# Optimization experiments

Measured on AMD Instinct MI355X. Metric: run time of the kernel, lower is better.

Reference implementation:

```python
import jax, jax.numpy as jnp
import numpy as np


def setup_inputs() -> dict:
    B, L, D, M, S = 4, 1024, 1024, 16, 8
    key = jax.random.key(0)
    ks = jax.random.split(key, 12)
    sd = 0.02
    inp = {
        "hid": jax.random.normal(ks[0], (B, L, D), jnp.float32),
        "src_hid": jax.random.normal(ks[1], (B, L, D), jnp.float32),
        "sp_width": jax.random.randint(ks[2], (B, L), 0, 9),
        "max_sp_len": S,
        "attention_mask": jnp.ones((B, L), bool),
        "src_mask": jnp.ones((B, L), bool),
        # span-start attention (1 head): query/key linears + relative-key embedding table
        "wq_st": sd * jax.random.normal(ks[3], (D, D), jnp.float32),
        "bq_st": jnp.zeros((D,), jnp.float32),
        "wk_st": sd * jax.random.normal(ks[4], (D, D), jnp.float32),
        "bk_st": jnp.zeros((D,), jnp.float32),
        "rel_st": sd * jax.random.normal(ks[5], (2 * M + 1, D), jnp.float32),
        # span-end attention
        "wq_ed": sd * jax.random.normal(ks[6], (D, D), jnp.float32),
        "bq_ed": jnp.zeros((D,), jnp.float32),
        "wk_ed": sd * jax.random.normal(ks[7], (D, D), jnp.float32),
        "bk_ed": jnp.zeros((D,), jnp.float32),
        "rel_ed": sd * jax.random.normal(ks[8], (2 * M + 1, D), jnp.float32),
        # sp_emb: Linear(2D -> D), stored as [2D, D] (x @ W + b)
        "sp_w": sd * jax.random.normal(ks[9], (2 * D, D), jnp.float32),
        "sp_b": jnp.zeros((D,), jnp.float32),
    }
    return inp


def reference(hid, src_hid, sp_width, max_sp_len, attention_mask, src_mask,
              wq_st, bq_st, wk_st, bk_st, rel_st,
              wq_ed, bq_ed, wk_ed, bk_ed, rel_ed, sp_w, sp_b):
    B, L, D = hid.shape
    scale = 1.0 / jnp.sqrt(jnp.float32(D))
    M = (rel_st.shape[0] - 1) // 2
    pos = jnp.arange(L)
    rel_idx = jnp.clip(pos[None, :] - pos[:, None], -M, M) + M          # [L,L]
    rel_idx_b = jnp.broadcast_to(rel_idx[None], (B, L, L))

    amask = (src_mask[:, :, None] & attention_mask[:, None, :]).astype(jnp.float32)  # [B,Lq,Lk]
    attn_w0 = amask / jnp.clip(jnp.sum(amask, 2, keepdims=True), 1e-6)

    def attn(query, wq, bq, wk, bk, rel_tab, mask):
        # single-head relative-position attention; returns attention weights [B,L,L]
        q = (query @ wq + bq) * scale                                   # [B,L,D]
        k = hid @ wk + bk                                               # [B,L,D]
        sc = jnp.einsum('bqd,bkd->bqk', q, k)
        # q . rel_emb[rel_idx[q_pos,k_pos]]: contract with table then gather (avoids [L,L,D])
        rel_sc = jnp.take_along_axis(jnp.einsum('bqd,rd->bqr', q, rel_tab), rel_idx_b, axis=2)
        sc = jnp.where(mask > 0, sc + rel_sc, -1e18)
        return jax.nn.softmax(sc, axis=-1)

    def upd(attn_w, hidp):
        # weighted sum of hid + linear + relu (dropout is identity in eval)
        hidc = jnp.einsum('bqk,bkd->bqd', attn_w, hid)
        return jax.nn.relu(jnp.concatenate([hidp, hidc], axis=2) @ sp_w + sp_b)

    sts, eds, masks = [attn_w0], [attn_w0], []
    hid1, hid2 = src_hid, src_hid
    for i in range(max_sp_len):
        m = (i < sp_width).astype(jnp.float32)                          # [B,L]
        masks.append(m)
        mask_i = m[:, :, None] * amask                                  # [B,L,L]
        hid1 = upd(sts[-1], hid1)
        sts.append(attn(hid1, wq_st, bq_st, wk_st, bk_st, rel_st, mask_i))
        hid2 = upd(eds[-1], hid2)
        eds.append(attn(hid2, wq_ed, bq_ed, wk_ed, bk_ed, rel_ed, mask_i))

    return (jnp.stack(sts[1:], -2),   # [B,L,S,L]
            jnp.stack(eds[1:], -2),   # [B,L,S,L]
            jnp.stack(masks, -1))     # [B,L,S]
```

## Files before the change

### kernel.cpp

```cpp
#include <hip/hip_runtime.h>

typedef unsigned short u16;
typedef __attribute__((ext_vector_type(8))) short bh8;
typedef __attribute__((ext_vector_type(4))) float f4;

__device__ __forceinline__ u16 f2b(float x){
  union { float f; unsigned u; } c; c.f = x;
  unsigned r = (c.u + 0x7FFFu + ((c.u >> 16) & 1u)) >> 16;
  return (u16)r;
}
__device__ __forceinline__ float b2f(u16 h){
  union { unsigned u; float f; } c; c.u = ((unsigned)h) << 16; return c.f;
}
__device__ __forceinline__ void gload16(const void* g, void* l){
  __builtin_amdgcn_global_load_lds((const __attribute__((address_space(1))) void*)g,
                                   (__attribute__((address_space(3))) void*)l, 16, 0, 0);
}


__global__ __launch_bounds__(256) void convall_k(const float* __restrict__ hid,
                                                 const float* __restrict__ wq0, const float* __restrict__ wq1,
                                                 const float* __restrict__ wk0, const float* __restrict__ wk1,
                                                 u16* __restrict__ hidB, u16* __restrict__ wqB, u16* __restrict__ wkB){
  long i = (long)blockIdx.x*256 + threadIdx.x;
  const float* src; u16* dst; long off;
  if      (i < 4194304L){ src = hid; dst = hidB;           off = i; }
  else if (i < 5242880L){ src = wq0; dst = wqB;            off = i - 4194304L; }
  else if (i < 6291456L){ src = wq1; dst = wqB + 1048576;  off = i - 5242880L; }
  else if (i < 7340032L){ src = wk0; dst = wkB;            off = i - 6291456L; }
  else                  { src = wk1; dst = wkB + 1048576;  off = i - 7340032L; }
  dst[off] = f2b(src[off]);
}

__global__ __launch_bounds__(256) void uniform_k(const int* __restrict__ spw, float* __restrict__ out){
  int blk = blockIdx.x;
  int s = blk >> 12, bl = blk & 4095;
  int w = spw[bl];
  if (w >= 8) return;
  float* base = out + (size_t)s*33554432ull + (size_t)bl*8192;
  f4 t = {0.0009765625f, 0.0009765625f, 0.0009765625f, 0.0009765625f};
  for (int i = w; i < 8; i++)
    ((f4*)(base + (size_t)i*1024))[threadIdx.x] = t;
}

__global__ __launch_bounds__(256) void trans_k(const float* __restrict__ in, u16* __restrict__ out,
                                               int R, int C){
  __shared__ u16 t[32][33];
  int bx = blockIdx.x*32, by = blockIdx.y*32;
  int tx = threadIdx.x & 31, ty = threadIdx.x >> 5;
  #pragma unroll
  for (int j = 0; j < 32; j += 8) t[ty+j][tx] = f2b(in[(size_t)(by+ty+j)*C + bx+tx]);
  __syncthreads();
  #pragma unroll
  for (int j = 0; j < 32; j += 8) out[(size_t)(bx+ty+j)*R + by+tx] = t[tx][ty+j];
}

__global__ __launch_bounds__(256) void sort_k(const int* __restrict__ spw, int* __restrict__ perm,
                                              int* __restrict__ cnt, float* __restrict__ mout){
  int b = blockIdx.x, t = threadIdx.x;
  __shared__ int hist[9], start[9];
  if (t < 9) hist[t] = 0;
  __syncthreads();
  for (int l = t; l < 1024; l += 256) atomicAdd(&hist[spw[b*1024 + l]], 1);
  __syncthreads();
  if (t == 0){
    int acc = 0;
    for (int w = 8; w >= 0; w--){ start[w] = acc; acc += hist[w]; }
  }
  __syncthreads();
  if (t < 8) cnt[b*8 + t] = start[t];
  __syncthreads();
  for (int l = t; l < 1024; l += 256){
    int w = spw[b*1024 + l];
    float* mo = mout + ((size_t)b*1024 + l)*8;
    #pragma unroll
    for (int i = 0; i < 8; i++) mo[i] = (i < w) ? 1.0f : 0.0f;
    int pos = atomicAdd(&start[w], 1);
    perm[b*1024 + pos] = l;
  }
}

__global__ __launch_bounds__(256) void gather_k(const float* __restrict__ srch, const int* __restrict__ perm,
                                                u16* __restrict__ hb){
  int blk = blockIdx.x;
  int z = blk >> 10, c = blk & 1023, b = z & 3;
  int ro = perm[b*1024 + c];
  const float* src = srch + ((size_t)b*1024 + ro)*1024;
  u16* dst = hb + ((size_t)z*1024 + c)*1024;
  for (int d = threadIdx.x; d < 1024; d += 256) dst[d] = f2b(src[d]);
}

__global__ __launch_bounds__(256) void wrt_k(const float* __restrict__ wq0, const float* __restrict__ wq1,
                                             const float* __restrict__ rel0, const float* __restrict__ rel1,
                                             u16* __restrict__ Mx){
  long idx = (long)blockIdx.x*256 + threadIdx.x;
  if (idx >= 2L*33*1024) return;
  int s = idx >= 33*1024; long loc = idx - (s ? 33*1024 : 0);
  int r = (int)(loc >> 10), e = (int)(loc & 1023);
  const float* wqrow = (s ? wq1 : wq0) + (size_t)e*1024;
  const float* rel = (s ? rel1 : rel0) + (size_t)r*1024;
  float acc = 0.0f;
  #pragma unroll 4
  for (int k = 0; k < 1024; k++) acc += wqrow[k]*rel[k];
  u16 v = f2b(acc*0.03125f);
  size_t o = (size_t)(1024 + r)*1024 + e;
  #pragma unroll
  for (int b = 0; b < 4; b++)
    Mx[(size_t)(s*4 + b)*1179648 + o] = v;
}

__global__ __launch_bounds__(256) void dots_k(const float* __restrict__ wq0, const float* __restrict__ wq1,
                                              const float* __restrict__ wk0, const float* __restrict__ wk1,
                                              const float* __restrict__ bq0, const float* __restrict__ bq1,
                                              const float* __restrict__ bk0, const float* __restrict__ bk1,
                                              const float* __restrict__ rel0, const float* __restrict__ rel1,
                                              float* __restrict__ ubuf, float* __restrict__ c0buf,
                                              float* __restrict__ bqbk, float* __restrict__ cba){
  int row = blockIdx.x*4 + (threadIdx.x >> 6);
  int lane = threadIdx.x & 63;
  if (row >= 4164) return;
  const float *a, *v;
  int kind = 0, oi = 0, br_s = 0, br_r = 0;
  if      (row < 1024){ a = wk0 + (size_t)row*1024; v = bq0; oi = row; }
  else if (row < 2048){ a = wk1 + (size_t)(row-1024)*1024; v = bq1; oi = row; }
  else if (row < 3072){ a = wq0 + (size_t)(row-2048)*1024; v = bk0; kind = 1; oi = row-2048; }
  else if (row < 4096){ a = wq1 + (size_t)(row-3072)*1024; v = bk1; kind = 1; oi = row-3072+1024; }
  else if (row < 4162){ int idx = row-4096; br_s = idx/33; br_r = idx%33;
                        a = (br_s ? rel1 : rel0) + (size_t)br_r*1024; v = br_s ? bq1 : bq0; kind = 2; }
  else                { int s2 = row-4162; a = s2 ? bq1 : bq0; v = s2 ? bk1 : bk0; kind = 3; oi = s2; }
  const f4* ap = (const f4*)a;
  const f4* vp = (const f4*)v;
  float acc = 0.0f;
  #pragma unroll
  for (int p = 0; p < 4; p++){
    f4 x = ap[lane + 64*p], y = vp[lane + 64*p];
    acc += x[0]*y[0] + x[1]*y[1] + x[2]*y[2] + x[3]*y[3];
  }
  #pragma unroll
  for (int off = 32; off > 0; off >>= 1) acc += __shfl_xor(acc, off, 64);
  if (lane == 0){
    if (kind == 0) ubuf[oi] = acc;
    else if (kind == 1) c0buf[oi] = acc;
    else if (kind == 2){
      float w = acc*0.03125f;
      for (int b = 0; b < 4; b++) cba[(br_s*4 + b)*1152 + 1024 + br_r] = w;
    } else bqbk[oi] = acc;
  }
}

__global__ __launch_bounds__(256) void cba_k(const float* __restrict__ hid, const float* __restrict__ u,
                                             const float* __restrict__ bqbk, float* __restrict__ cba){
  int row = blockIdx.x*4 + (threadIdx.x >> 6);
  int lane = threadIdx.x & 63;
  int z = row >> 10, l = row & 1023, b = z & 3, s = z >> 2;
  const f4* hp = (const f4*)(hid + ((size_t)b*1024 + l)*1024);
  const f4* up = (const f4*)(u + s*1024);
  float acc = 0.0f;
  #pragma unroll
  for (int p = 0; p < 4; p++){
    f4 a = hp[lane + 64*p], c = up[lane + 64*p];
    acc += a[0]*c[0] + a[1]*c[1] + a[2]*c[2] + a[3]*c[3];
  }
  #pragma unroll
  for (int off = 32; off > 0; off >>= 1) acc += __shfl_xor(acc, off, 64);
  if (!lane) cba[z*1152 + l] = (acc + bqbk[s])*0.03125f;
}

__global__ __launch_bounds__(256) void meanh2_k(const u16* __restrict__ H2T, float* __restrict__ mh){
  int row = blockIdx.x*4 + (threadIdx.x >> 6);
  int lane = threadIdx.x & 63;
  const u16* p = H2T + (size_t)row*1024 + lane*16;
  float s = 0.0f;
  #pragma unroll
  for (int j = 0; j < 16; j++) s += b2f(p[j]);
  #pragma unroll
  for (int off = 32; off > 0; off >>= 1) s += __shfl_xor(s, off, 64);
  if (lane == 0) mh[row] = s * 0.0009765625f;
}

__global__ __launch_bounds__(256) void softmax_k(const u16* __restrict__ scB, float* __restrict__ outF,
                                                 u16* __restrict__ attnP, const float* __restrict__ qrelb,
                                                 const int* __restrict__ cnt, const int* __restrict__ perm,
                                                 int iter){
  int z = blockIdx.x >> 10, c = blockIdx.x & 1023;
  int s = z >> 2, b = z & 3;
  if (c >= cnt[b*8 + iter]) return;
  int ro = perm[b*1024 + c];
  __shared__ float qr[33];
  __shared__ float red[8];
  if (threadIdx.x < 33) qr[threadIdx.x] = qrelb[((size_t)z*1024 + c)*33 + threadIdx.x];
  __syncthreads();
  const u16* sc = scB + ((size_t)z*1024 + c)*1024;
  float* po = outF + (size_t)s*33554432ull + (((size_t)(b*1024 + ro))*8 + (size_t)iter)*1024;
  u16* pr = attnP + ((size_t)z*1024 + c)*1024;
  int t = threadIdx.x;
  float v[4]; float mx = -1e30f;
  #pragma unroll
  for (int j = 0; j < 4; j++){
    int col = t + j*256;
    int d = col - ro; d = d < -16 ? -16 : (d > 16 ? 16 : d);
    v[j] = b2f(sc[col]) + qr[d + 16];
    mx = fmaxf(mx, v[j]);
  }
  #pragma unroll
  for (int off = 32; off > 0; off >>= 1) mx = fmaxf(mx, __shfl_xor(mx, off, 64));
  int wv = t >> 6, ln = t & 63;
  if (ln == 0) red[wv] = mx;
  __syncthreads();
  mx = fmaxf(fmaxf(red[0], red[1]), fmaxf(red[2], red[3]));
  float sm = 0.0f;
  #pragma unroll
  for (int j = 0; j < 4; j++){ v[j] = __expf(v[j] - mx); sm += v[j]; }
  #pragma unroll
  for (int off = 32; off > 0; off >>= 1) sm += __shfl_xor(sm, off, 64);
  if (ln == 0) red[4 + wv] = sm;
  __syncthreads();
  sm = red[4] + red[5] + red[6] + red[7];
  float inv = 1.0f / sm;
  #pragma unroll
  for (int j = 0; j < 4; j++){
    float pv = v[j] * inv;
    po[t + j*256] = pv;
    pr[t + j*256] = f2b(pv);
  }
}

template<int MODE>
__global__ __launch_bounds__(256) void gemm_k(
    const u16* __restrict__ A_, const u16* __restrict__ B_,
    const u16* __restrict__ A2_, const u16* __restrict__ B2_,
    const float* __restrict__ e0, const float* __restrict__ e1,
    u16* __restrict__ outB, float* __restrict__ qrelb,
    const int* __restrict__ cnt, int iter)
{
  const int z = blockIdx.z;
  const int s = (MODE == 1) ? 0 : (z >> 2);
  const int b = (MODE == 1) ? z : (z & 3);
  const size_t LD = 1024*1024;
  const int bm = blockIdx.y*128, bn = blockIdx.x*128;

  int cntv = 1024;
  if constexpr (MODE == 2 || MODE == 4){
    cntv = cnt[b*8 + iter];
    if (bm >= cntv) return;
  }

  const u16 *A1, *B1, *A2, *B2;
  int lda1 = 1024, ldb1 = 1024, lda2 = 1024, ldb2 = 1024, K = 1024, K1 = 1024;

  if constexpr (MODE == 0){ A1 = A_ + (size_t)z*LD; B1 = B_ + (size_t)z*LD; A2=A1; B2=B1; }
  else if constexpr (MODE == 1){ A1 = A_ + 1024; lda1 = 2048; B1 = B_ + (size_t)z*LD; A2=A1; B2=B1; lda2=lda1; }
  else if constexpr (MODE == 2){
    A1 = A_ + (size_t)z*LD; B1 = B_ + (size_t)b*LD;
    A2 = A2_ + (size_t)z*LD; B2 = B2_; ldb2 = 2048;
    if (iter == 0){ K = 1024; K1 = 0; } else { K = 2048; K1 = 1024; }
  }
  else if constexpr (MODE == 3){ A1 = A_ + (size_t)b*LD; B1 = B_ + (size_t)s*LD; A2=A1; B2=B1; }
  else { A1 = A_ + (size_t)z*LD; B1 = B_ + (size_t)z*1179648; A2=A1; B2=B1; }

  __shared__ __align__(16) u16 lA[16384];
  __shared__ __align__(16) u16 lB[16384];
  const int tid = threadIdx.x, wv = tid >> 6, lane = tid & 63;
  const int wr = (wv >> 1)*64, wc = (wv & 1)*64;
  const int fr = lane & 15, kh = lane >> 4;
  const int stRow = (lane >> 2);
  const int ssw  = ((lane >> 2) & 3) ^ ((lane >> 4) & 3);
  const int stCe = ((lane & 3) ^ ssw)*8;
  const int fsw  = (fr & 3) ^ ((fr >> 2) & 3);
  const int rdSl = (kh ^ fsw)*8;

  auto stage = [&](int bufsel, int k0s){
    const u16 *As, *Bs; int kk, la, lb;
    if (k0s < K1){ As = A1; Bs = B1; kk = k0s; la = lda1; lb = ldb1; }
    else         { As = A2; Bs = B2; kk = k0s - K1; la = lda2; lb = ldb2; }
    #pragma unroll
    for (int c = 0; c < 4; c++){
      const int n = wv*4 + c;
      const int h = n >> 3;
      const int rl = (n & 7)*16 + stRow;
      const int ke = kk + h*32 + stCe;
      gload16(As + (size_t)(bm + rl)*la + ke, (char*)lA + bufsel*16384 + n*1024);
      gload16(Bs + (size_t)(bn + rl)*lb + ke, (char*)lB + bufsel*16384 + n*1024);
    }
  };

  f4 acc[4][4];
  #pragma unroll
  for (int i = 0; i < 4; i++)
    #pragma unroll
    for (int j = 0; j < 4; j++)
      acc[i][j] = f4{0.f, 0.f, 0.f, 0.f};

  stage(0, 0);
  stage(1, 64);

  int cur = 0;
  for (int k0 = 0; k0 < K; k0 += 64){
    if (k0 + 64 < K) asm volatile("s_waitcnt vmcnt(8)" ::: "memory");
    else             asm volatile("s_waitcnt vmcnt(0)" ::: "memory");
    __builtin_amdgcn_s_barrier();
    asm volatile("" ::: "memory");
    const u16* bufA = lA + cur*8192;
    const u16* bufB = lB + cur*8192;
    bh8 af[2][4], bfr[2][4];
    #pragma unroll
    for (int h = 0; h < 2; h++){
      #pragma unroll
      for (int i = 0; i < 4; i++){
        af[h][i]  = *(const bh8*)&bufA[h*4096 + (wr + i*16 + fr)*32 + rdSl];
        bfr[h][i] = *(const bh8*)&bufB[h*4096 + (wc + i*16 + fr)*32 + rdSl];
      }
    }
    if (k0 + 128 < K){
      asm volatile("s_waitcnt lgkmcnt(0)" ::: "memory");
      __builtin_amdgcn_sched_barrier(0);
      __builtin_amdgcn_s_barrier();
      asm volatile("" ::: "memory");
      stage(cur, k0 + 128);
    }
    __builtin_amdgcn_s_setprio(1);
    #pragma unroll
    for (int h = 0; h < 2; h++)
      #pragma unroll
      for (int i = 0; i < 4; i++)
        #pragma unroll
        for (int j = 0; j < 4; j++)
          acc[i][j] = __builtin_amdgcn_mfma_f32_16x16x32_bf16(af[h][i], bfr[h][j], acc[i][j], 0, 0, 0);
    __builtin_amdgcn_s_setprio(0);
    cur ^= 1;
  }

  const int rw = (lane >> 4)*4, cl = lane & 15;
  #pragma unroll
  for (int i = 0; i < 4; i++){
    #pragma unroll
    for (int r = 0; r < 4; r++){
      const int row = bm + wr + i*16 + rw + r;
      if constexpr (MODE == 2 || MODE == 4){ if (row >= cntv) continue; }
      #pragma unroll
      for (int j = 0; j < 4; j++){
        const int col = bn + wc + j*16 + cl;
        float v = acc[i][j][r];
        if constexpr (MODE == 0 || MODE == 1){
          outB[(size_t)z*LD + (size_t)row*1024 + col] = f2b(v);
        } else if constexpr (MODE == 2){
          v += e0[col];
          if (e1) v += e1[b*1024 + col];
          v = fmaxf(v, 0.0f);
          outB[(size_t)z*LD + (size_t)row*1024 + col] = f2b(v);
        } else if constexpr (MODE == 3){
          outB[(size_t)z*1179648 + (size_t)row*1024 + col] = f2b((v + e0[s*1024 + col])*0.03125f);
        } else {
          v += e0[z*1152 + col];
          if (col < 1024){
            outB[((size_t)z*1024 + row)*1024 + col] = f2b(v);
          } else {
            int rr = col - 1024;
            if (rr < 33) qrelb[((size_t)z*1024 + row)*33 + rr] = v;
          }
        }
      }
    }
  }
}


extern "C" void kernel_launch(void* const* d_in, const int* in_sizes, int n_in,
                              void* d_out, int out_size, void* d_ws, size_t ws_size,
                              hipStream_t stream)
{
  const float* hid    = (const float*)d_in[0];
  const float* srch   = (const float*)d_in[1];
  const int*   spw    = (const int*)d_in[2];
  const float* wq_st  = (const float*)d_in[6];
  const float* bq_st  = (const float*)d_in[7];
  const float* wk_st  = (const float*)d_in[8];
  const float* bk_st  = (const float*)d_in[9];
  const float* rel_st = (const float*)d_in[10];
  const float* wq_ed  = (const float*)d_in[11];
  const float* bq_ed  = (const float*)d_in[12];
  const float* wk_ed  = (const float*)d_in[13];
  const float* bk_ed  = (const float*)d_in[14];
  const float* rel_ed = (const float*)d_in[15];
  const float* sp_w   = (const float*)d_in[16];
  const float* sp_b   = (const float*)d_in[17];
  float* out = (float*)d_out;

  const size_t LD = 1024*1024;
  char* p = (char*)d_ws;
  u16* hidB  = (u16*)p; p += 4*LD*2;
  u16* wqB   = (u16*)p; p += 2*LD*2;
  u16* wkB   = (u16*)p; p += 2*LD*2;
  u16* spwT  = (u16*)p; p += 2*LD*2;
  u16* WT    = (u16*)p; p += 2*LD*2;
  u16* H2T   = (u16*)p; p += 4*LD*2;
  u16* Mx    = (u16*)p; p += 8ull*1179648*2;
  u16* attnP = (u16*)p; p += 8*LD*2;
  u16* hbufA = (u16*)p; p += 8*LD*2;
  u16* hbufB = (u16*)p; p += 8*LD*2;
  u16* scB   = (u16*)p; p += 8*LD*2;
  float* qrelb  = (float*)p; p += 8*1024*33*4;
  float* cba    = (float*)p; p += 8*1152*4;
  float* ubuf   = (float*)p; p += 2048*4;
  float* c0buf  = (float*)p; p += 2048*4;
  float* bqbk   = (float*)p; p += 64;
  float* meanH2 = (float*)p; p += 4*1024*4;
  int*   perm   = (int*)p;   p += 4*1024*4;
  int*   cnt    = (int*)p;   p += 1024;

  const dim3 t256(256);

  convall_k<<<32768, t256, 0, stream>>>(hid, wq_st, wq_ed, wk_st, wk_ed, hidB, wqB, wkB);
  sort_k<<<4, t256, 0, stream>>>(spw, perm, cnt, out + 67108864ull);
  gather_k<<<8192, t256, 0, stream>>>(srch, perm, hbufA);
  uniform_k<<<8192, t256, 0, stream>>>(spw, out);
  trans_k<<<dim3(32,64), t256, 0, stream>>>(sp_w, spwT, 2048, 1024);
  wrt_k<<<264, t256, 0, stream>>>(wq_st, wq_ed, rel_st, rel_ed, Mx);
  dots_k<<<1041, t256, 0, stream>>>(wq_st, wq_ed, wk_st, wk_ed, bq_st, bq_ed, bk_st, bk_ed,
                                    rel_st, rel_ed, ubuf, c0buf, bqbk, cba);
  cba_k<<<2048, t256, 0, stream>>>(hid, ubuf, bqbk, cba);

  gemm_k<0><<<dim3(8,8,2), t256, 0, stream>>>(wqB, wkB, nullptr, nullptr, nullptr, nullptr,
                                              WT, nullptr, nullptr, 0);
  gemm_k<3><<<dim3(8,8,8), t256, 0, stream>>>(hidB, WT, nullptr, nullptr, c0buf, nullptr,
                                              Mx, nullptr, nullptr, 0);
  gemm_k<1><<<dim3(8,8,4), t256, 0, stream>>>(spwT, hidB, nullptr, nullptr, nullptr, nullptr,
                                              H2T, nullptr, nullptr, 0);
  meanh2_k<<<1024, t256, 0, stream>>>(H2T, meanH2);

  u16* hp = hbufA; u16* hn = hbufB;
  for (int i = 0; i < 8; i++){
    gemm_k<2><<<dim3(8,8,8), t256, 0, stream>>>(attnP, H2T, hp, spwT, sp_b,
                                                (i == 0) ? meanH2 : nullptr,
                                                hn, nullptr, cnt, i);
    gemm_k<4><<<dim3(9,8,8), t256, 0, stream>>>(hn, Mx, nullptr, nullptr, cba, nullptr,
                                                scB, qrelb, cnt, i);
    softmax_k<<<8192, t256, 0, stream>>>(scB, out, attnP, qrelb, cnt, perm, i);
    u16* tmp = hp; hp = hn; hn = tmp;
  }
}
```

Measured before the change: 927.0 us.

## Split GEMM k-step into halves and fuse uniform fill into softmax

The GEMM main loop now loads the two k-halves of the LDS tile separately and runs MFMAs on the first half while the second half's LDS reads are in flight. The barrier and the next-stage prefetch now sit between the two MFMA halves, so LDS reads overlap more with compute. Separately, the uniform-fill kernel now only handles rows whose span width is zero. For other rows, softmax writes the uniform tail rows at the iteration where the span ends. This removes most of a standalone write pass, but puts scattered extra stores into softmax and adds an unconditional barrier per k-step.

Measured after the change: 965.6 us. 4.2% more time.

```diff
diff --git a/kernel.cpp b/kernel.cpp
--- a/kernel.cpp
+++ b/kernel.cpp
@@ -32,15 +32,17 @@
   dst[off] = f2b(src[off]);
 }
 
-__global__ __launch_bounds__(256) void uniform_k(const int* __restrict__ spw, float* __restrict__ out){
-  int blk = blockIdx.x;
-  int s = blk >> 12, bl = blk & 4095;
-  int w = spw[bl];
-  if (w >= 8) return;
-  float* base = out + (size_t)s*33554432ull + (size_t)bl*8192;
+__global__ __launch_bounds__(256) void uniform0_k(const int* __restrict__ spw, float* __restrict__ out){
+  int bl = blockIdx.x;
+  if (spw[bl] != 0) return;
   f4 t = {0.0009765625f, 0.0009765625f, 0.0009765625f, 0.0009765625f};
-  for (int i = w; i < 8; i++)
-    ((f4*)(base + (size_t)i*1024))[threadIdx.x] = t;
+  float* b0 = out + (size_t)bl*8192;
+  float* b1 = out + 33554432ull + (size_t)bl*8192;
+  #pragma unroll
+  for (int i = 0; i < 8; i++){
+    ((f4*)(b0 + (size_t)i*1024))[threadIdx.x] = t;
+    ((f4*)(b1 + (size_t)i*1024))[threadIdx.x] = t;
+  }
 }
 
 __global__ __launch_bounds__(256) void trans_k(const float* __restrict__ in, u16* __restrict__ out,
@@ -181,7 +183,7 @@
 __global__ __launch_bounds__(256) void softmax_k(const u16* __restrict__ scB, float* __restrict__ outF,
                                                  u16* __restrict__ attnP, const float* __restrict__ qrelb,
                                                  const int* __restrict__ cnt, const int* __restrict__ perm,
-                                                 int iter){
+                                                 const int* __restrict__ spw, int iter){
   int z = blockIdx.x >> 10, c = blockIdx.x & 1023;
   int s = z >> 2, b = z & 3;
   if (c >= cnt[b*8 + iter]) return;
@@ -222,6 +224,12 @@
     float pv = v[j] * inv;
     po[t + j*256] = pv;
     pr[t + j*256] = f2b(pv);
+  }
+  int w = spw[b*1024 + ro];
+  if (iter == w - 1 && w < 8){
+    f4 u = {0.0009765625f, 0.0009765625f, 0.0009765625f, 0.0009765625f};
+    for (int j = 1; j <= 7 - iter; j++)
+      ((f4*)(po + (size_t)j*1024))[t] = u;
   }
 }
 
@@ -304,28 +312,36 @@
     const u16* bufB = lB + cur*8192;
     bh8 af[2][4], bfr[2][4];
     #pragma unroll
-    for (int h = 0; h < 2; h++){
+    for (int i = 0; i < 4; i++){
+      af[0][i]  = *(const bh8*)&bufA[(wr + i*16 + fr)*32 + rdSl];
+      bfr[0][i] = *(const bh8*)&bufB[(wc + i*16 + fr)*32 + rdSl];
+    }
+    __builtin_amdgcn_sched_barrier(0);
+    #pragma unroll
+    for (int i = 0; i < 4; i++){
+      af[1][i]  = *(const bh8*)&bufA[4096 + (wr + i*16 + fr)*32 + rdSl];
+      bfr[1][i] = *(const bh8*)&bufB[4096 + (wc + i*16 + fr)*32 + rdSl];
+    }
+    asm volatile("s_waitcnt lgkmcnt(8)" ::: "memory");
+    __builtin_amdgcn_sched_barrier(0);
+    __builtin_amdgcn_s_setprio(1);
+    #pragma unroll
+    for (int i = 0; i < 4; i++)
       #pragma unroll
-      for (int i = 0; i < 4; i++){
-        af[h][i]  = *(const bh8*)&bufA[h*4096 + (wr + i*16 + fr)*32 + rdSl];
-        bfr[h][i] = *(const bh8*)&bufB[h*4096 + (wc + i*16 + fr)*32 + rdSl];
-      }
-    }
-    if (k0 + 128 < K){
-      asm volatile("s_waitcnt lgkmcnt(0)" ::: "memory");
-      __builtin_amdgcn_sched_barrier(0);
-      __builtin_amdgcn_s_barrier();
-      asm volatile("" ::: "memory");
-      stage(cur, k0 + 128);
-    }
+      for (int j = 0; j < 4; j++)
+        acc[i][j] = __builtin_amdgcn_mfma_f32_16x16x32_bf16(af[0][i], bfr[0][j], acc[i][j], 0, 0, 0);
+    __builtin_amdgcn_s_setprio(0);
+    asm volatile("s_waitcnt lgkmcnt(0)" ::: "memory");
+    __builtin_amdgcn_sched_barrier(0);
+    __builtin_amdgcn_s_barrier();
+    asm volatile("" ::: "memory");
+    if (k0 + 128 < K) stage(cur, k0 + 128);
     __builtin_amdgcn_s_setprio(1);
     #pragma unroll
-    for (int h = 0; h < 2; h++)
+    for (int i = 0; i < 4; i++)
       #pragma unroll
-      for (int i = 0; i < 4; i++)
-        #pragma unroll
-        for (int j = 0; j < 4; j++)
-          acc[i][j] = __builtin_amdgcn_mfma_f32_16x16x32_bf16(af[h][i], bfr[h][j], acc[i][j], 0, 0, 0);
+      for (int j = 0; j < 4; j++)
+        acc[i][j] = __builtin_amdgcn_mfma_f32_16x16x32_bf16(af[1][i], bfr[1][j], acc[i][j], 0, 0, 0);
     __builtin_amdgcn_s_setprio(0);
     cur ^= 1;
   }
@@ -413,7 +429,7 @@
   convall_k<<<32768, t256, 0, stream>>>(hid, wq_st, wq_ed, wk_st, wk_ed, hidB, wqB, wkB);
   sort_k<<<4, t256, 0, stream>>>(spw, perm, cnt, out + 67108864ull);
   gather_k<<<8192, t256, 0, stream>>>(srch, perm, hbufA);
-  uniform_k<<<8192, t256, 0, stream>>>(spw, out);
+  uniform0_k<<<4096, t256, 0, stream>>>(spw, out);
   trans_k<<<dim3(32,64), t256, 0, stream>>>(sp_w, spwT, 2048, 1024);
   wrt_k<<<264, t256, 0, stream>>>(wq_st, wq_ed, rel_st, rel_ed, Mx);
   dots_k<<<1041, t256, 0, stream>>>(wq_st, wq_ed, wk_st, wk_ed, bq_st, bq_ed, bk_st, bk_ed,
@@ -435,7 +451,7 @@
                                                 hn, nullptr, cnt, i);
     gemm_k<4><<<dim3(9,8,8), t256, 0, stream>>>(hn, Mx, nullptr, nullptr, cba, nullptr,
                                                 scB, qrelb, cnt, i);
-    softmax_k<<<8192, t256, 0, stream>>>(scB, out, attnP, qrelb, cnt, perm, i);
+    softmax_k<<<8192, t256, 0, stream>>>(scB, out, attnP, qrelb, cnt, perm, spw, i);
     u16* tmp = hp; hp = hn; hn = tmp;
   }
 }
```
